# Performance work log

Hardware: AMD Instinct MI355X
Metric: run time of the kernel (lower is better)

The kernel has to match this reference:

```python
import jax, jax.numpy as jnp
import numpy as np

N_NODES = 100000
N_EDGES = 1600000
NODE_DIM = 128
EDGE_DIM = 32
GLOBAL_DIM = 64
HIDDEN_DIM = 256
N_GRAPHS = 512
IN_DIM = NODE_DIM + EDGE_DIM + GLOBAL_DIM  # 224


def setup_inputs() -> dict:
    key = jax.random.key(0)
    ks = jax.random.split(key, 10)
    x = jax.random.normal(ks[0], (N_NODES, NODE_DIM), dtype=jnp.float32)
    edge_index = jax.random.randint(ks[1], (2, N_EDGES), 0, N_NODES, dtype=jnp.int64)
    edge_attr = jax.random.normal(ks[2], (N_EDGES, EDGE_DIM), dtype=jnp.float32)
    u = jax.random.normal(ks[3], (N_GRAPHS, GLOBAL_DIM), dtype=jnp.float32)
    batch = jnp.sort(jax.random.randint(ks[4], (N_NODES,), 0, N_GRAPHS, dtype=jnp.int64))
    s1 = 1.0 / np.sqrt(IN_DIM)
    s2 = 1.0 / np.sqrt(HIDDEN_DIM)
    W1 = jax.random.uniform(ks[5], (IN_DIM, HIDDEN_DIM), jnp.float32, -s1, s1)
    b1 = jnp.zeros((HIDDEN_DIM,), jnp.float32)
    W2 = jax.random.uniform(ks[6], (HIDDEN_DIM, HIDDEN_DIM), jnp.float32, -s2, s2)
    b2 = jnp.zeros((HIDDEN_DIM,), jnp.float32)
    W3 = jax.random.uniform(ks[7], (HIDDEN_DIM, GLOBAL_DIM), jnp.float32, -s2, s2)
    b3 = jnp.zeros((GLOBAL_DIM,), jnp.float32)
    return {"x": x, "edge_index": edge_index, "edge_attr": edge_attr, "u": u,
            "batch": batch, "W1": W1, "b1": b1, "W2": W2, "b2": b2, "W3": W3, "b3": b3}


def _scatter_mean(vals, seg_ids, num_segments):
    # vals: [M, D], seg_ids: [M] -> [num_segments, D]
    sums = jax.ops.segment_sum(vals, seg_ids, num_segments=num_segments)
    cnt = jax.ops.segment_sum(jnp.ones((vals.shape[0],), vals.dtype), seg_ids,
                              num_segments=num_segments)
    return sums / jnp.maximum(cnt, 1.0)[:, None]


def reference(x, edge_index, edge_attr, u, batch, W1, b1, W2, b2, W3, b3):
    B = u.shape[0]
    node_mean = _scatter_mean(x, batch, B)                      # [B, node_dim]
    edge_seg = batch[edge_index[0]]                             # [E]
    edge_mean = _scatter_mean(edge_attr, edge_seg, B)           # [B, edge_dim]
    out = jnp.concatenate([node_mean, edge_mean, u], axis=1)    # [B, in_dim]
    h = jax.nn.relu(out @ W1 + b1)
    h = jax.nn.relu(h @ W2 + b2)
    return h @ W3 + b3                                          # [B, global_dim]
```

## Files before the change

### kernel.cpp

```cpp
#include <hip/hip_runtime.h>
#include <hip/hip_bf16.h>

#define N_NODES    100000
#define N_EDGES    1600000
#define NODE_DIM   128
#define EDGE_DIM   32
#define GLOBAL_DIM 64
#define HIDDEN_DIM 256
#define N_GRAPHS   512
#define IN_DIM     224
#define ROW33      33

#define EDGE_BLKS  512
#define EDGE_CH    (N_EDGES / EDGE_BLKS)
#define SLOTSZ     (N_GRAPHS * ROW33)
#define GPB        2

#define FXS   1048576.0f
#define FXINV (1.0f / 1048576.0f)

#define WS_NSUM   0
#define WS_NCNT   (WS_NSUM + N_GRAPHS * NODE_DIM)
#define WS_ESLOT  (WS_NCNT + N_GRAPHS)

__global__ __launch_bounds__(1024) void bulk(const float* __restrict__ eattr,
                                             const int* __restrict__ eidx,
                                             const float* __restrict__ x,
                                             const int* __restrict__ batch,
                                             int* __restrict__ eslot,
                                             float* __restrict__ nsum,
                                             float* __restrict__ ncnt) {
    __shared__ int ssum[SLOTSZ];
    const int t = threadIdx.x;

    if (blockIdx.x < EDGE_BLKS) {
        for (int i = t; i < SLOTSZ; i += 1024) ssum[i] = 0;
        __syncthreads();

        const float4* eattr4 = reinterpret_cast<const float4*>(eattr);
        const int p = t & 3;
        const int e1 = blockIdx.x * EDGE_CH + EDGE_CH;
        int e = blockIdx.x * EDGE_CH + (t >> 2);

        int s_nxt = 0;
        float4 va_nxt = float4{0.f, 0.f, 0.f, 0.f}, vb_nxt = va_nxt;
        if (e < e1) {
            s_nxt  = batch[eidx[e]];
            va_nxt = eattr4[(size_t)e * 8 + p * 2];
            vb_nxt = eattr4[(size_t)e * 8 + p * 2 + 1];
        }

        for (; e < e1; e += 256) {
            const int s = s_nxt;
            const float4 va = va_nxt, vb = vb_nxt;
            const int en = e + 256;
            if (en < e1) {
                s_nxt  = batch[eidx[en]];
                va_nxt = eattr4[(size_t)en * 8 + p * 2];
                vb_nxt = eattr4[(size_t)en * 8 + p * 2 + 1];
            }
            const int b = s * ROW33 + p * 8;
            atomicAdd(&ssum[b + 0], __float2int_rn(va.x * FXS));
            atomicAdd(&ssum[b + 1], __float2int_rn(va.y * FXS));
            atomicAdd(&ssum[b + 2], __float2int_rn(va.z * FXS));
            atomicAdd(&ssum[b + 3], __float2int_rn(va.w * FXS));
            atomicAdd(&ssum[b + 4], __float2int_rn(vb.x * FXS));
            atomicAdd(&ssum[b + 5], __float2int_rn(vb.y * FXS));
            atomicAdd(&ssum[b + 6], __float2int_rn(vb.z * FXS));
            atomicAdd(&ssum[b + 7], __float2int_rn(vb.w * FXS));
            if (p == 0) atomicAdd(&ssum[s * ROW33 + 32], 1);
        }
        __syncthreads();

        int* gs = eslot + (size_t)blockIdx.x * SLOTSZ;
        for (int i = t; i < SLOTSZ; i += 1024) gs[i] = ssum[i];
    } else {
        const int g = blockIdx.x - EDGE_BLKS;
        __shared__ int sb[2];
        if (t < 2) {
            const int target = g + t;
            int lo = 0, hi = N_NODES;
            while (lo < hi) {
                const int mid = (lo + hi) >> 1;
                if (batch[mid] < target) lo = mid + 1; else hi = mid;
            }
            sb[t] = lo;
        }
        __syncthreads();
        const int s0 = sb[0], e0 = sb[1];

        const int dq = t & 31;
        const int off = t >> 5;
        float4 a0 = float4{0.f, 0.f, 0.f, 0.f}, a1 = a0;
        int r = s0 + off;
        for (; r + 32 < e0; r += 64) {
            const float4 v0 = *reinterpret_cast<const float4*>(x + (size_t)(r     ) * NODE_DIM + dq * 4);
            const float4 v1 = *reinterpret_cast<const float4*>(x + (size_t)(r + 32) * NODE_DIM + dq * 4);
            a0.x += v0.x; a0.y += v0.y; a0.z += v0.z; a0.w += v0.w;
            a1.x += v1.x; a1.y += v1.y; a1.z += v1.z; a1.w += v1.w;
        }
        for (; r < e0; r += 32) {
            const float4 v = *reinterpret_cast<const float4*>(x + (size_t)r * NODE_DIM + dq * 4);
            a0.x += v.x; a0.y += v.y; a0.z += v.z; a0.w += v.w;
        }
        a0.x += a1.x; a0.y += a1.y; a0.z += a1.z; a0.w += a1.w;

        float4* part4 = reinterpret_cast<float4*>(ssum);
        part4[t] = a0;
        __syncthreads();
        if (t < 32) {
            float4 s = float4{0.f, 0.f, 0.f, 0.f};
#pragma unroll 32
            for (int k = 0; k < 32; ++k) {
                const float4 v = part4[t + 32 * k];
                s.x += v.x; s.y += v.y; s.z += v.z; s.w += v.w;
            }
            reinterpret_cast<float4*>(nsum)[(size_t)g * 32 + t] = s;
        }
        if (t == 0) ncnt[g] = fmaxf((float)(e0 - s0), 1.f);
    }
}

__global__ __launch_bounds__(256) void finalize_mlp(const float* __restrict__ nsum,
                                                    const float* __restrict__ ncnt,
                                                    const int* __restrict__ eslot,
                                                    const float* __restrict__ u,
                                                    const float* __restrict__ W1, const float* __restrict__ b1,
                                                    const float* __restrict__ W2, const float* __restrict__ b2,
                                                    const float* __restrict__ W3, const float* __restrict__ b3,
                                                    float* __restrict__ out) {
    const int g0 = blockIdx.x * GPB;
    const int t = threadIdx.x;
    __shared__ float fs[GPB * IN_DIM];
    __shared__ long long redll[256];
    __shared__ long long redcnt[8];
    __shared__ float h[GPB][HIDDEN_DIM];
    __shared__ float h2[GPB][HIDDEN_DIM];
    __shared__ float red[GPB][256];
    __shared__ float s_ecnt[GPB];

    {
        const int col = t & 63, part = t >> 6;
        const int g = col >> 5, d = col & 31;
        long long s = 0;
#pragma unroll 8
        for (int sl = part * 128; sl < part * 128 + 128; ++sl)
            s += eslot[(size_t)sl * SLOTSZ + (size_t)(g0 + g) * ROW33 + d];
        redll[t] = s;
    }
    if (t < 8) {
        const int g = t & 1, part = t >> 1;
        long long c = 0;
#pragma unroll 8
        for (int sl = part * 128; sl < part * 128 + 128; ++sl)
            c += eslot[(size_t)sl * SLOTSZ + (size_t)(g0 + g) * ROW33 + 32];
        redcnt[t] = c;
    }
    __syncthreads();
    if (t < GPB)
        s_ecnt[t] = fmaxf((float)(redcnt[t] + redcnt[t + 2] + redcnt[t + 4] + redcnt[t + 6]), 1.f);

    {
        const int g = t >> 7, d = t & 127;
        fs[g * IN_DIM + d] = nsum[(size_t)(g0 + g) * NODE_DIM + d] / ncnt[g0 + g];
    }
    __syncthreads();
    if (t < 64) {
        const long long tot = redll[t] + redll[t + 64] + redll[t + 128] + redll[t + 192];
        const int g = t >> 5, d = t & 31;
        fs[g * IN_DIM + NODE_DIM + d] = ((float)tot * FXINV) / s_ecnt[g];
    } else if (t < 192) {
        const int i = t - 64, g = i >> 6, c = i & 63;
        fs[g * IN_DIM + NODE_DIM + EDGE_DIM + c] = u[(size_t)(g0 + g) * GLOBAL_DIM + c];
    }
    __syncthreads();

    float acc0, acc1;
    const float bb1 = b1[t];
    acc0 = acc1 = bb1;
    for (int k = 0; k < IN_DIM; ++k) {
        const float w = W1[k * HIDDEN_DIM + t];
        acc0 = fmaf(fs[k], w, acc0);
        acc1 = fmaf(fs[IN_DIM + k], w, acc1);
    }
    h[0][t] = fmaxf(acc0, 0.f); h[1][t] = fmaxf(acc1, 0.f);
    __syncthreads();

    const float bb2 = b2[t];
    acc0 = acc1 = bb2;
    for (int k = 0; k < HIDDEN_DIM; ++k) {
        const float w = W2[k * HIDDEN_DIM + t];
        acc0 = fmaf(h[0][k], w, acc0);
        acc1 = fmaf(h[1][k], w, acc1);
    }
    h2[0][t] = fmaxf(acc0, 0.f); h2[1][t] = fmaxf(acc1, 0.f);
    __syncthreads();

    const int c3 = t & 63, q = t >> 6;
    acc0 = acc1 = 0.f;
    for (int k = q * 64; k < q * 64 + 64; ++k) {
        const float w = W3[k * GLOBAL_DIM + c3];
        acc0 = fmaf(h2[0][k], w, acc0);
        acc1 = fmaf(h2[1][k], w, acc1);
    }
    red[0][t] = acc0; red[1][t] = acc1;
    __syncthreads();
    if (t < GPB * GLOBAL_DIM) {
        const int g = t >> 6, c = t & 63;
        out[(size_t)(g0 + g) * GLOBAL_DIM + c] = red[g][c] + red[g][c + 64] +
                                                 red[g][c + 128] + red[g][c + 192] + b3[c];
    }
}

extern "C" void kernel_launch(void* const* d_in, const int* in_sizes, int n_in,
                              void* d_out, int out_size, void* d_ws, size_t ws_size,
                              hipStream_t stream) {
    const float* x         = (const float*)d_in[0];
    const int*   edge_idx  = (const int*)d_in[1];
    const float* edge_attr = (const float*)d_in[2];
    const float* u         = (const float*)d_in[3];
    const int*   batch     = (const int*)d_in[4];
    const float* W1 = (const float*)d_in[5];
    const float* b1 = (const float*)d_in[6];
    const float* W2 = (const float*)d_in[7];
    const float* b2 = (const float*)d_in[8];
    const float* W3 = (const float*)d_in[9];
    const float* b3 = (const float*)d_in[10];
    float* out = (float*)d_out;

    int* ws32 = (int*)d_ws;
    float* nsum  = (float*)(ws32 + WS_NSUM);
    float* ncnt  = (float*)(ws32 + WS_NCNT);
    int*   eslot = ws32 + WS_ESLOT;

    bulk<<<EDGE_BLKS + N_GRAPHS, 1024, 0, stream>>>(edge_attr, edge_idx, x, batch,
                                                    eslot, nsum, ncnt);
    finalize_mlp<<<N_GRAPHS / GPB, 256, 0, stream>>>(nsum, ncnt, eslot, u,
                                                     W1, b1, W2, b2, W3, b3, out);
}
```

Baseline: 95.46 us.

## Halve edge blocks, use 8 threads per edge, and prefetch indices two iterations ahead

The edge-reduction phase now uses half as many blocks, each covering twice as many edges, so there are fewer per-block partial slots to write and then sum in the MLP kernel. Each edge is split across 8 lanes loading one float4 each instead of 4 lanes loading two. The edge-index load is software-pipelined two iterations ahead so the dependent batch lookup overlaps the atomics. The cost is less parallelism in the edge phase, more LDS atomic contention per block, and more loop iterations per thread.

```diff
diff --git a/kernel.cpp b/kernel.cpp
--- a/kernel.cpp
+++ b/kernel.cpp
@@ -11,7 +11,7 @@
 #define IN_DIM     224
 #define ROW33      33
 
-#define EDGE_BLKS  512
+#define EDGE_BLKS  256
 #define EDGE_CH    (N_EDGES / EDGE_BLKS)
 #define SLOTSZ     (N_GRAPHS * ROW33)
 #define GPB        2
@@ -38,37 +38,37 @@
         __syncthreads();
 
         const float4* eattr4 = reinterpret_cast<const float4*>(eattr);
-        const int p = t & 3;
+        const int p = t & 7;
         const int e1 = blockIdx.x * EDGE_CH + EDGE_CH;
-        int e = blockIdx.x * EDGE_CH + (t >> 2);
-
-        int s_nxt = 0;
-        float4 va_nxt = float4{0.f, 0.f, 0.f, 0.f}, vb_nxt = va_nxt;
+        int e = blockIdx.x * EDGE_CH + (t >> 3);
+
+        int s_c = 0, idx_n = 0;
+        float4 v_c = float4{0.f, 0.f, 0.f, 0.f};
         if (e < e1) {
-            s_nxt  = batch[eidx[e]];
-            va_nxt = eattr4[(size_t)e * 8 + p * 2];
-            vb_nxt = eattr4[(size_t)e * 8 + p * 2 + 1];
-        }
-
-        for (; e < e1; e += 256) {
-            const int s = s_nxt;
-            const float4 va = va_nxt, vb = vb_nxt;
-            const int en = e + 256;
+            const int idx0 = eidx[e];
+            if (e + 128 < e1) idx_n = eidx[e + 128];
+            s_c = batch[idx0];
+            v_c = eattr4[(size_t)e * 8 + p];
+        }
+
+        for (; e < e1; e += 128) {
+            const int en = e + 128;
+            int s_n = 0;
+            float4 v_n = float4{0.f, 0.f, 0.f, 0.f};
             if (en < e1) {
-                s_nxt  = batch[eidx[en]];
-                va_nxt = eattr4[(size_t)en * 8 + p * 2];
-                vb_nxt = eattr4[(size_t)en * 8 + p * 2 + 1];
+                s_n = batch[idx_n];
+                v_n = eattr4[(size_t)en * 8 + p];
             }
-            const int b = s * ROW33 + p * 8;
-            atomicAdd(&ssum[b + 0], __float2int_rn(va.x * FXS));
-            atomicAdd(&ssum[b + 1], __float2int_rn(va.y * FXS));
-            atomicAdd(&ssum[b + 2], __float2int_rn(va.z * FXS));
-            atomicAdd(&ssum[b + 3], __float2int_rn(va.w * FXS));
-            atomicAdd(&ssum[b + 4], __float2int_rn(vb.x * FXS));
-            atomicAdd(&ssum[b + 5], __float2int_rn(vb.y * FXS));
-            atomicAdd(&ssum[b + 6], __float2int_rn(vb.z * FXS));
-            atomicAdd(&ssum[b + 7], __float2int_rn(vb.w * FXS));
-            if (p == 0) atomicAdd(&ssum[s * ROW33 + 32], 1);
+            const int idx_nn = (e + 256 < e1) ? eidx[e + 256] : 0;
+
+            const int b = s_c * ROW33 + p * 4;
+            atomicAdd(&ssum[b + 0], __float2int_rn(v_c.x * FXS));
+            atomicAdd(&ssum[b + 1], __float2int_rn(v_c.y * FXS));
+            atomicAdd(&ssum[b + 2], __float2int_rn(v_c.z * FXS));
+            atomicAdd(&ssum[b + 3], __float2int_rn(v_c.w * FXS));
+            if (p == 0) atomicAdd(&ssum[s_c * ROW33 + 32], 1);
+
+            s_c = s_n; v_c = v_n; idx_n = idx_nn;
         }
         __syncthreads();
 
@@ -144,7 +144,7 @@
         const int g = col >> 5, d = col & 31;
         long long s = 0;
 #pragma unroll 8
-        for (int sl = part * 128; sl < part * 128 + 128; ++sl)
+        for (int sl = part * 64; sl < part * 64 + 64; ++sl)
             s += eslot[(size_t)sl * SLOTSZ + (size_t)(g0 + g) * ROW33 + d];
         redll[t] = s;
     }
@@ -152,7 +152,7 @@
         const int g = t & 1, part = t >> 1;
         long long c = 0;
 #pragma unroll 8
-        for (int sl = part * 128; sl < part * 128 + 128; ++sl)
+        for (int sl = part * 64; sl < part * 64 + 64; ++sl)
             c += eslot[(size_t)sl * SLOTSZ + (size_t)(g0 + g) * ROW33 + 32];
         redcnt[t] = c;
     }
```

New measurement: 80.71 us. 1.18x faster.
